# Optimization experiments

Hardware: AMD Instinct MI355X
Metric: run time of the kernel (lower is better)

## Reference

```python
import jax, jax.numpy as jnp
import numpy as np
import math

B, S, D, H, KV, HD = 2, 2048, 2048, 32, 8, 64
N_REP = H // KV


def setup_inputs() -> dict:
    key = jax.random.key(0)
    ks = jax.random.split(key, 6)
    x = jax.random.normal(ks[0], (B, S, D), jnp.float32)
    # torch Linear weights, stored as [in, out] for x @ w
    wq = jax.random.normal(ks[1], (D, H * HD), jnp.float32) * 0.02
    wk = jax.random.normal(ks[2], (D, KV * HD), jnp.float32) * 0.02
    wv = jax.random.normal(ks[3], (D, KV * HD), jnp.float32) * 0.02
    wo = jax.random.normal(ks[4], (H * HD, D), jnp.float32) * 0.02
    # rotary angle table: theta[t, j] = t / 10000^(2j/head_dim)
    inv_freq = 1.0 / (10000.0 ** (jnp.arange(0, HD, 2, dtype=jnp.float32) / HD))
    freqs = jnp.arange(S, dtype=jnp.float32)[:, None] * inv_freq[None, :]  # [S, HD//2]
    mask = jnp.triu(jnp.full((S, S), -1e9, dtype=jnp.float32), k=1)
    return {"x": x, "wq": wq, "wk": wk, "wv": wv, "wo": wo,
            "freqs": freqs, "mask": mask, "start_pos": 0}


def _apply_rope(t, cos, sin):
    # t: [b, s, h, d]; pairs are adjacent (llama complex convention)
    b, s, h, d = t.shape
    t2 = t.reshape(b, s, h, d // 2, 2)
    tr, ti = t2[..., 0], t2[..., 1]
    c = cos[None, :, None, :]
    sn = sin[None, :, None, :]
    out_r = tr * c - ti * sn
    out_i = tr * sn + ti * c
    return jnp.stack([out_r, out_i], axis=-1).reshape(b, s, h, d)


def reference(x, wq, wk, wv, wo, freqs, mask, start_pos):
    bsz, seqlen, _ = x.shape
    cos, sin = jnp.cos(freqs), jnp.sin(freqs)
    xq = (x @ wq).reshape(bsz, seqlen, H, HD)
    xk = (x @ wk).reshape(bsz, seqlen, KV, HD)
    xv = (x @ wv).reshape(bsz, seqlen, KV, HD)
    xq = _apply_rope(xq, cos, sin)
    xk = _apply_rope(xk, cos, sin)
    # start_pos == 0 prefill: cache slice [:start_pos+seqlen] == fresh k/v
    keys = jnp.repeat(xk, N_REP, axis=2)    # [b, s, H, hd]
    values = jnp.repeat(xv, N_REP, axis=2)
    q = xq.transpose(0, 2, 1, 3)            # [b, H, s, hd]
    k = keys.transpose(0, 2, 1, 3)
    v = values.transpose(0, 2, 1, 3)
    scores = jnp.einsum('bhqd,bhkd->bhqk', q, k) / math.sqrt(HD)
    scores = scores + mask[None, None, :, :]
    probs = jax.nn.softmax(scores.astype(jnp.float32), axis=-1).astype(q.dtype)
    out = jnp.einsum('bhqk,bhkd->bhqd', probs, v)
    out = out.transpose(0, 2, 1, 3).reshape(bsz, seqlen, H * HD)
    return out @ wo
```

## Files before the change

### kernel.cpp

```cpp
#include <hip/hip_runtime.h>

typedef __attribute__((ext_vector_type(8))) __bf16 bf16x8;
typedef __attribute__((ext_vector_type(4)))  float f32x4;
typedef __attribute__((ext_vector_type(16))) float f32x16;

__device__ __forceinline__ unsigned short f2bfu(float x) {
  union { float f; unsigned u; } v; v.f = x;
  unsigned r = v.u + 0x7fffu + ((v.u >> 16) & 1u);
  return (unsigned short)(r >> 16);
}
__device__ __forceinline__ float bf2f(unsigned short u) {
  union { unsigned u; float f; } v; v.u = ((unsigned)u) << 16;
  return v.f;
}
__device__ __forceinline__ unsigned pkbf(float a, float b) {
  return (unsigned)f2bfu(a) | ((unsigned)f2bfu(b) << 16);
}
__device__ __forceinline__ void gload16(const void* g, void* l) {
  __builtin_amdgcn_global_load_lds((const __attribute__((address_space(1))) unsigned*)g,
                                   (__attribute__((address_space(3))) unsigned*)l, 16, 0, 0);
}
__device__ __forceinline__ bf16x8 mk8(unsigned a, unsigned b, unsigned c, unsigned d) {
  union { unsigned u[4]; bf16x8 v; } t;
  t.u[0] = a; t.u[1] = b; t.u[2] = c; t.u[3] = d; return t.v;
}

__global__ void cvt_kernel(const float* __restrict__ s, short* __restrict__ d, int n) {
  int i = (blockIdx.x * 256 + threadIdx.x) * 4;
  if (i >= n) return;
  float4 v = *(const float4*)(s + i);
  short4 o;
  o.x = (short)f2bfu(v.x); o.y = (short)f2bfu(v.y);
  o.z = (short)f2bfu(v.z); o.w = (short)f2bfu(v.w);
  *(short4*)(d + i) = o;
}

__global__ void transcvt_kernel(const float* __restrict__ src, short* __restrict__ dst,
                                int R, int C) {
  __shared__ __align__(16) float tl[64][65];
  int c0 = blockIdx.x * 64, r0 = blockIdx.y * 64;
  int t = threadIdx.x;
  int tr = t >> 4, tc = (t & 15) * 4;
#pragma unroll
  for (int i = 0; i < 4; i++) {
    int r = i * 16 + tr;
    float4 v = *(const float4*)(src + (size_t)(r0 + r) * C + c0 + tc);
    tl[r][tc] = v.x; tl[r][tc + 1] = v.y; tl[r][tc + 2] = v.z; tl[r][tc + 3] = v.w;
  }
  __syncthreads();
#pragma unroll
  for (int i = 0; i < 4; i++) {
    int cr = i * 16 + tr;
    short4 o;
    o.x = (short)f2bfu(tl[tc][cr]);
    o.y = (short)f2bfu(tl[tc + 1][cr]);
    o.z = (short)f2bfu(tl[tc + 2][cr]);
    o.w = (short)f2bfu(tl[tc + 3][cr]);
    *(short4*)(dst + (size_t)(c0 + cr) * R + r0 + tc) = o;
  }
}

__global__ void sincos_kernel(const float* __restrict__ freqs, float* __restrict__ ct,
                              float* __restrict__ st) {
  int i = blockIdx.x * 256 + threadIdx.x;
  float f = freqs[i];
  ct[i] = cosf(f);
  st[i] = sinf(f);
}

template <int OUTF32>
__global__ __launch_bounds__(256) void gemm_bt(const short* __restrict__ A,
                                               const short* __restrict__ Bt,
                                               void* __restrict__ C, int M, int N, int K) {
  __shared__ __align__(16) short Al[128 * 32];
  __shared__ __align__(16) short Bl[128 * 32];
  const int t = threadIdx.x, lane = t & 63, w = t >> 6;
  const int m0 = blockIdx.x * 128, n0 = blockIdx.y * 128;
  const int wm = (w & 1) * 64, wn = (w >> 1) * 64;
  f32x4 acc[4][4];
#pragma unroll
  for (int i = 0; i < 4; i++)
#pragma unroll
    for (int j = 0; j < 4; j++)
#pragma unroll
      for (int r = 0; r < 4; r++) acc[i][j][r] = 0.f;

  const int sr = t >> 2;
  const int ss = t & 3;
  const int ldsbase = w * 512;

  for (int k0 = 0; k0 < K; k0 += 32) {
    __syncthreads();
#pragma unroll
    for (int p = 0; p < 2; p++) {
      int r = p * 64 + sr;
      int c = 8 * (ss ^ ((r >> 1) & 3));
      gload16(A + (size_t)(m0 + r) * K + k0 + c, &Al[p * 2048 + ldsbase]);
      gload16(Bt + (size_t)(n0 + r) * K + k0 + c, &Bl[p * 2048 + ldsbase]);
    }
    __syncthreads();
    bf16x8 af[4], bg[4];
#pragma unroll
    for (int i = 0; i < 4; i++) {
      int ra = wm + i * 16 + (lane & 15);
      int sa = (lane >> 4) ^ ((ra >> 1) & 3);
      af[i] = *(const bf16x8*)(&Al[ra * 32 + sa * 8]);
      int rb = wn + i * 16 + (lane & 15);
      int sb = (lane >> 4) ^ ((rb >> 1) & 3);
      bg[i] = *(const bf16x8*)(&Bl[rb * 32 + sb * 8]);
    }
#pragma unroll
    for (int i = 0; i < 4; i++)
#pragma unroll
      for (int j = 0; j < 4; j++)
        acc[i][j] = __builtin_amdgcn_mfma_f32_16x16x32_bf16(af[i], bg[j], acc[i][j], 0, 0, 0);
  }
  const int cr = (lane >> 4) * 4, cc = lane & 15;
#pragma unroll
  for (int i = 0; i < 4; i++)
#pragma unroll
    for (int j = 0; j < 4; j++)
#pragma unroll
      for (int r = 0; r < 4; r++) {
        size_t idx = (size_t)(m0 + wm + i * 16 + cr + r) * N + (n0 + wn + j * 16 + cc);
        if (OUTF32) ((float*)C)[idx] = acc[i][j][r];
        else        ((short*)C)[idx] = (short)f2bfu(acc[i][j][r]);
      }
}

__global__ void rope_kernel(short* __restrict__ qkv, const float* __restrict__ ct,
                            const float* __restrict__ st) {
  int idx = blockIdx.x * 256 + threadIdx.x;
  const int PQ = 4096 * 1024;
  int row, col, i;
  if (idx < PQ) {
    row = idx >> 10; int p = idx & 1023; int h = p >> 5; i = p & 31;
    col = h * 64 + 2 * i;
  } else {
    int k = idx - PQ; row = k >> 8; int p = k & 255; int kvh = p >> 5; i = p & 31;
    col = 2048 + kvh * 64 + 2 * i;
  }
  int s = row & 2047;
  unsigned* ptr = (unsigned*)(qkv + (size_t)row * 3072 + col);
  unsigned v = *ptr;
  float tr = bf2f((unsigned short)(v & 0xffff));
  float ti = bf2f((unsigned short)(v >> 16));
  float c = ct[(s << 5) + i], sn = st[(s << 5) + i];
  *ptr = pkbf(tr * c - ti * sn, tr * sn + ti * c);
}

__global__ void transv_kernel(const short* __restrict__ qkv, short* __restrict__ vt) {
  __shared__ __align__(16) short tl[64][72];
  int st0 = blockIdx.x * 64;
  int bkv = blockIdx.y; int b = bkv >> 3, kv = bkv & 7;
  int t = threadIdx.x;
  int rr = t >> 3, c8 = (t & 7) * 8;
#pragma unroll
  for (int i = 0; i < 2; i++) {
    int sl = i * 32 + rr;
    bf16x8 v = *(const bf16x8*)(qkv + (size_t)(b * 2048 + st0 + sl) * 3072 + 2560 + kv * 64 + c8);
    union { bf16x8 v; short s[8]; } u; u.v = v;
#pragma unroll
    for (int j = 0; j < 8; j++) tl[sl][c8 + j] = u.s[j];
  }
  __syncthreads();
#pragma unroll
  for (int i = 0; i < 2; i++) {
    int dl = i * 32 + rr;
    union { bf16x8 v; short s[8]; } o;
#pragma unroll
    for (int j = 0; j < 8; j++) o.s[j] = tl[c8 + j][dl];
    *(bf16x8*)(vt + ((size_t)(bkv * 64 + dl)) * 2048 + st0 + c8) = o.v;
  }
}

__global__ __launch_bounds__(256) void attn_kernel(const short* __restrict__ qkv,
                                                   const short* __restrict__ vt,
                                                   short* __restrict__ attn) {
  const int S = 2048, NC = 3072;
  __shared__ __align__(16) short kl[32 * 64];
  __shared__ __align__(16) short vl[64 * 32];
  __shared__ __align__(16) short ol[4][32 * 72];

  const int qb = blockIdx.x * 128;
  const int h = blockIdx.y, b = blockIdx.z;
  const int kvh = h >> 2;
  const int t = threadIdx.x, lane = t & 63, w = t >> 6;
  const int q0 = qb + w * 32;
  const int qc = lane & 31, hi = lane >> 5;
  const int qg = q0 + qc;

  bf16x8 bq[4];
  {
    const short* qp = qkv + (size_t)(b * S + qg) * NC + h * 64 + hi * 8;
#pragma unroll
    for (int kk = 0; kk < 4; kk++) bq[kk] = *(const bf16x8*)(qp + kk * 16);
  }

  f32x16 ot0, ot1;
#pragma unroll
  for (int r = 0; r < 16; r++) { ot0[r] = 0.f; ot1[r] = 0.f; }
  float m = -1e30f, l = 0.f;

  const int kr = w * 8 + (lane >> 3), sk = lane & 7;
  const short* kbase = qkv + (size_t)(b * S + kr) * NC + 2048 + kvh * 64 + 8 * (sk ^ (kr & 7));
  const int dv = w * 16 + (lane >> 2), sv = lane & 3;
  const short* vbase = vt + ((size_t)((b * 8 + kvh) * 64 + dv)) * S + 8 * (sv ^ ((dv >> 1) & 3));

  const int nt = (qb >> 5) + 4;
  for (int tile = 0; tile < nt; ++tile) {
    const int s0 = tile * 32;
    __syncthreads();
    gload16(kbase + (size_t)s0 * NC, &kl[w * 512]);
    gload16(vbase + s0, &vl[w * 512]);
    __syncthreads();

    f32x16 cs;
#pragma unroll
    for (int r = 0; r < 16; r++) cs[r] = 0.f;
    const int krow = lane & 31;
#pragma unroll
    for (int kk = 0; kk < 4; kk++) {
      int slot = (2 * kk + hi) ^ (krow & 7);
      bf16x8 ak = *(const bf16x8*)(&kl[krow * 64 + slot * 8]);
      cs = __builtin_amdgcn_mfma_f32_32x32x16_bf16(ak, bq[kk], cs, 0, 0, 0);
    }

    float e[16];
    const bool notfull = (s0 + 31 > q0);
#pragma unroll
    for (int r = 0; r < 16; r++) {
      float sv_ = cs[r] * 0.18033688011112042f;
      if (notfull) {
        int kgl = s0 + (r & 3) + 8 * (r >> 2) + 4 * hi;
        if (kgl > qg) sv_ = -1e30f;
      }
      e[r] = sv_;
    }
    float mx = e[0];
#pragma unroll
    for (int r = 1; r < 16; r++) mx = fmaxf(mx, e[r]);
    mx = fmaxf(mx, __shfl_xor(mx, 32, 64));
    float mn = fmaxf(m, mx);
    float rf = exp2f(m - mn);
    m = mn;
    float p[16]; float ls = 0.f;
#pragma unroll
    for (int r = 0; r < 16; r++) { p[r] = exp2f(e[r] - mn); ls += p[r]; }
    l = l * rf + ls;
#pragma unroll
    for (int r = 0; r < 16; r++) { ot0[r] *= rf; ot1[r] *= rf; }

    unsigned x[8], y[8];
#pragma unroll
    for (int j = 0; j < 8; j++) x[j] = pkbf(p[2 * j], p[2 * j + 1]);
#pragma unroll
    for (int j = 0; j < 8; j++) y[j] = (unsigned)__shfl_xor((int)x[j], 32, 64);
    bf16x8 pb0 = hi ? mk8(y[2], y[3], x[2], x[3]) : mk8(x[0], x[1], y[0], y[1]);
    bf16x8 pb1 = hi ? mk8(y[6], y[7], x[6], x[7]) : mk8(x[4], x[5], y[4], y[5]);

    const int dl = lane & 31;
#pragma unroll
    for (int ks = 0; ks < 2; ks++) {
      bf16x8 pb = ks ? pb1 : pb0;
#pragma unroll
      for (int dh = 0; dh < 2; dh++) {
        int d = dh * 32 + dl;
        int slot = (2 * ks + hi) ^ ((d >> 1) & 3);
        bf16x8 av = *(const bf16x8*)(&vl[d * 32 + slot * 8]);
        if (dh == 0) ot0 = __builtin_amdgcn_mfma_f32_32x32x16_bf16(av, pb, ot0, 0, 0, 0);
        else         ot1 = __builtin_amdgcn_mfma_f32_32x32x16_bf16(av, pb, ot1, 0, 0, 0);
      }
    }
  }

  float lt = l + __shfl_xor(l, 32, 64);
  float inv = 1.0f / lt;
#pragma unroll
  for (int dh = 0; dh < 2; dh++) {
#pragma unroll
    for (int j = 0; j < 8; j++) {
      int d = ((2 * j) & 3) + 8 * ((2 * j) >> 2) + 4 * hi + 32 * dh;
      float a = (dh ? ot1[2 * j] : ot0[2 * j]) * inv;
      float bb = (dh ? ot1[2 * j + 1] : ot0[2 * j + 1]) * inv;
      *(unsigned*)(&ol[w][qc * 72 + d]) = pkbf(a, bb);
    }
  }
  __syncthreads();
  const int qr = lane >> 1, part = lane & 1;
  short* og = attn + (size_t)(b * S + q0 + qr) * 2048 + h * 64 + part * 32;
  const short* ip = &ol[w][qr * 72 + part * 32];
#pragma unroll
  for (int i2 = 0; i2 < 4; i2++) *(bf16x8*)(og + i2 * 8) = *(const bf16x8*)(ip + i2 * 8);
}

extern "C" void kernel_launch(void* const* d_in, const int* in_sizes, int n_in,
                              void* d_out, int out_size, void* d_ws, size_t ws_size,
                              hipStream_t stream) {
  (void)in_sizes; (void)n_in; (void)out_size; (void)ws_size;
  const float* x     = (const float*)d_in[0];
  const float* wq    = (const float*)d_in[1];
  const float* wk    = (const float*)d_in[2];
  const float* wv    = (const float*)d_in[3];
  const float* wo    = (const float*)d_in[4];
  const float* freqs = (const float*)d_in[5];

  char* ws = (char*)d_ws;
  short* qkv  = (short*)(ws + 0);
  short* vtb  = (short*)(ws + 25165824);
  short* xb   = (short*)(ws + 29360128);
  short* attn = xb;
  short* wT   = (short*)(ws + 46137344);
  float* ct   = (float*)(ws + 58720256);
  float* st   = (float*)(ws + 58982400);

  cvt_kernel<<<8192, 256, 0, stream>>>(x, xb, 8388608);
  transcvt_kernel<<<dim3(32, 32), 256, 0, stream>>>(wq, wT, 2048, 2048);
  transcvt_kernel<<<dim3(8, 32), 256, 0, stream>>>(wk, wT + (size_t)2048 * 2048, 2048, 512);
  transcvt_kernel<<<dim3(8, 32), 256, 0, stream>>>(wv, wT + (size_t)2560 * 2048, 2048, 512);
  sincos_kernel<<<256, 256, 0, stream>>>(freqs, ct, st);
  gemm_bt<0><<<dim3(32, 24), 256, 0, stream>>>(xb, wT, qkv, 4096, 3072, 2048);
  transcvt_kernel<<<dim3(32, 32), 256, 0, stream>>>(wo, wT, 2048, 2048);
  rope_kernel<<<20480, 256, 0, stream>>>(qkv, ct, st);
  transv_kernel<<<dim3(32, 16), 256, 0, stream>>>(qkv, vtb);
  attn_kernel<<<dim3(16, 32, 2), 256, 0, stream>>>(qkv, vtb, attn);
  gemm_bt<1><<<dim3(32, 16), 256, 0, stream>>>(attn, wT, d_out, 4096, 2048, 2048);
}
```

Baseline: 473.9 us.

## Double-buffer 64-key K/V tiles in attention with prescaled Q and reversed block order

The attention loop now processes 64 keys per iteration instead of 32 and double-buffers K/V tiles in shared memory, so the next tile's global-to-LDS loads overlap with the current tile's MFMA work. The softmax scale is folded into Q once at load time rather than applied per score. Query blocks are launched in reverse order so the longest causal blocks start first, and bf16 packing uses the native conversion. The cost is more LDS per block, which may lower occupancy, and scaling Q before the bf16 round adds a small rounding change.

```diff
diff --git a/kernel.cpp b/kernel.cpp
--- a/kernel.cpp
+++ b/kernel.cpp
@@ -15,6 +15,11 @@
 }
 __device__ __forceinline__ unsigned pkbf(float a, float b) {
   return (unsigned)f2bfu(a) | ((unsigned)f2bfu(b) << 16);
+}
+__device__ __forceinline__ unsigned pk2(float a, float b) {
+  union { __bf16 h[2]; unsigned u; } t;
+  t.h[0] = (__bf16)a; t.h[1] = (__bf16)b;
+  return t.u;
 }
 __device__ __forceinline__ void gload16(const void* g, void* l) {
   __builtin_amdgcn_global_load_lds((const __attribute__((address_space(1))) unsigned*)g,
@@ -178,11 +183,9 @@
                                                    const short* __restrict__ vt,
                                                    short* __restrict__ attn) {
   const int S = 2048, NC = 3072;
-  __shared__ __align__(16) short kl[32 * 64];
-  __shared__ __align__(16) short vl[64 * 32];
-  __shared__ __align__(16) short ol[4][32 * 72];
-
-  const int qb = blockIdx.x * 128;
+  __shared__ __align__(16) short sh[2][2][64 * 64];
+
+  const int qb = (int)(gridDim.x - 1 - blockIdx.x) * 128;
   const int h = blockIdx.y, b = blockIdx.z;
   const int kvh = h >> 2;
   const int t = threadIdx.x, lane = t & 63, w = t >> 6;
@@ -193,8 +196,15 @@
   bf16x8 bq[4];
   {
     const short* qp = qkv + (size_t)(b * S + qg) * NC + h * 64 + hi * 8;
-#pragma unroll
-    for (int kk = 0; kk < 4; kk++) bq[kk] = *(const bf16x8*)(qp + kk * 16);
+    const float SC = 0.18033688011112042f;
+#pragma unroll
+    for (int kk = 0; kk < 4; kk++) {
+      union { bf16x8 v; unsigned short s[8]; } u, o;
+      u.v = *(const bf16x8*)(qp + kk * 16);
+#pragma unroll
+      for (int j = 0; j < 8; j++) o.s[j] = f2bfu(bf2f(u.s[j]) * SC);
+      bq[kk] = o.v;
+    }
   }
 
   f32x16 ot0, ot1;
@@ -202,78 +212,115 @@
   for (int r = 0; r < 16; r++) { ot0[r] = 0.f; ot1[r] = 0.f; }
   float m = -1e30f, l = 0.f;
 
-  const int kr = w * 8 + (lane >> 3), sk = lane & 7;
-  const short* kbase = qkv + (size_t)(b * S + kr) * NC + 2048 + kvh * 64 + 8 * (sk ^ (kr & 7));
-  const int dv = w * 16 + (lane >> 2), sv = lane & 3;
-  const short* vbase = vt + ((size_t)((b * 8 + kvh) * 64 + dv)) * S + 8 * (sv ^ ((dv >> 1) & 3));
-
-  const int nt = (qb >> 5) + 4;
-  for (int tile = 0; tile < nt; ++tile) {
-    const int s0 = tile * 32;
+  const int r8 = lane >> 3, sl8 = lane & 7;
+  const int scol0 = 8 * (sl8 ^ ((r8 + w) & 7));
+  const int scol1 = 8 * (sl8 ^ ((r8 + 4 + w) & 7));
+  const short* kptr = qkv + (size_t)(b * S + w * 8 + r8) * NC + 2048 + kvh * 64;
+  const short* vptr = vt + (size_t)((b * 8 + kvh) * 64 + w * 8 + r8) * S;
+
+  const int nt = (qb >> 6) + 2;
+
+#define STAGE(tt, bb)                                                                   \
+  do {                                                                                  \
+    gload16(kptr + (size_t)((tt) * 64) * NC + scol0,        &sh[bb][0][(w * 8) * 64]);  \
+    gload16(kptr + (size_t)((tt) * 64 + 32) * NC + scol1,   &sh[bb][0][(32 + w * 8) * 64]); \
+    gload16(vptr + (size_t)(tt) * 64 + scol0,               &sh[bb][1][(w * 8) * 64]);  \
+    gload16(vptr + (size_t)32 * S + (tt) * 64 + scol1,      &sh[bb][1][(32 + w * 8) * 64]); \
+  } while (0)
+
+  STAGE(0, 0);
+  __syncthreads();
+
+  for (int tt = 0; tt < nt; ++tt) {
+    const int cur = tt & 1;
+    if (tt + 1 < nt) STAGE(tt + 1, cur ^ 1);
+    const int s0 = tt * 64;
+    const short* kb = &sh[cur][0][0];
+    const short* vb = &sh[cur][1][0];
+
+    f32x16 cs0, cs1;
+#pragma unroll
+    for (int r = 0; r < 16; r++) { cs0[r] = 0.f; cs1[r] = 0.f; }
+    const int kr0 = lane & 31, kr1 = kr0 + 32;
+    const int sw0 = (kr0 + (kr0 >> 3)) & 7, sw1 = (kr1 + (kr1 >> 3)) & 7;
+#pragma unroll
+    for (int kk = 0; kk < 4; kk++) {
+      bf16x8 a0 = *(const bf16x8*)(kb + kr0 * 64 + ((2 * kk + hi) ^ sw0) * 8);
+      cs0 = __builtin_amdgcn_mfma_f32_32x32x16_bf16(a0, bq[kk], cs0, 0, 0, 0);
+      bf16x8 a1 = *(const bf16x8*)(kb + kr1 * 64 + ((2 * kk + hi) ^ sw1) * 8);
+      cs1 = __builtin_amdgcn_mfma_f32_32x32x16_bf16(a1, bq[kk], cs1, 0, 0, 0);
+    }
+
+    if (s0 + 63 > q0) {
+      const int qrel = qg - s0;
+#pragma unroll
+      for (int r = 0; r < 16; r++) {
+        const int k0 = (r & 3) + 8 * (r >> 2) + 4 * hi;
+        if (k0 > qrel)      cs0[r] = -1e30f;
+        if (k0 + 32 > qrel) cs1[r] = -1e30f;
+      }
+    }
+
+    float mx = fmaxf(cs0[0], cs1[0]);
+#pragma unroll
+    for (int r = 1; r < 16; r++) mx = fmaxf(mx, fmaxf(cs0[r], cs1[r]));
+    mx = fmaxf(mx, __shfl_xor(mx, 32, 64));
+    const float mn = fmaxf(m, mx);
+    const float rf = exp2f(m - mn);
+    m = mn;
+    float ls = 0.f;
+#pragma unroll
+    for (int r = 0; r < 16; r++) { cs0[r] = exp2f(cs0[r] - mn); ls += cs0[r]; }
+#pragma unroll
+    for (int r = 0; r < 16; r++) { cs1[r] = exp2f(cs1[r] - mn); ls += cs1[r]; }
+    l = l * rf + ls;
+#pragma unroll
+    for (int r = 0; r < 16; r++) { ot0[r] *= rf; ot1[r] *= rf; }
+
+    unsigned x0[8], y0[8], x1[8], y1[8];
+#pragma unroll
+    for (int j = 0; j < 8; j++) x0[j] = pk2(cs0[2 * j], cs0[2 * j + 1]);
+#pragma unroll
+    for (int j = 0; j < 8; j++) y0[j] = (unsigned)__shfl_xor((int)x0[j], 32, 64);
+#pragma unroll
+    for (int j = 0; j < 8; j++) x1[j] = pk2(cs1[2 * j], cs1[2 * j + 1]);
+#pragma unroll
+    for (int j = 0; j < 8; j++) y1[j] = (unsigned)__shfl_xor((int)x1[j], 32, 64);
+    bf16x8 pb0 = hi ? mk8(y0[2], y0[3], x0[2], x0[3]) : mk8(x0[0], x0[1], y0[0], y0[1]);
+    bf16x8 pb1 = hi ? mk8(y0[6], y0[7], x0[6], x0[7]) : mk8(x0[4], x0[5], y0[4], y0[5]);
+    bf16x8 pb2 = hi ? mk8(y1[2], y1[3], x1[2], x1[3]) : mk8(x1[0], x1[1], y1[0], y1[1]);
+    bf16x8 pb3 = hi ? mk8(y1[6], y1[7], x1[6], x1[7]) : mk8(x1[4], x1[5], y1[4], y1[5]);
+
+    const int dl = lane & 31;
+    {
+      const int d = dl;
+      const int swd = (d + (d >> 3)) & 7;
+      bf16x8 v0 = *(const bf16x8*)(vb + d * 64 + ((0 + hi) ^ swd) * 8);
+      bf16x8 v1 = *(const bf16x8*)(vb + d * 64 + ((2 + hi) ^ swd) * 8);
+      bf16x8 v2 = *(const bf16x8*)(vb + d * 64 + ((4 + hi) ^ swd) * 8);
+      bf16x8 v3 = *(const bf16x8*)(vb + d * 64 + ((6 + hi) ^ swd) * 8);
+      ot0 = __builtin_amdgcn_mfma_f32_32x32x16_bf16(v0, pb0, ot0, 0, 0, 0);
+      ot0 = __builtin_amdgcn_mfma_f32_32x32x16_bf16(v1, pb1, ot0, 0, 0, 0);
+      ot0 = __builtin_amdgcn_mfma_f32_32x32x16_bf16(v2, pb2, ot0, 0, 0, 0);
+      ot0 = __builtin_amdgcn_mfma_f32_32x32x16_bf16(v3, pb3, ot0, 0, 0, 0);
+    }
+    {
+      const int d = 32 + dl;
+      const int swd = (d + (d >> 3)) & 7;
+      bf16x8 v0 = *(const bf16x8*)(vb + d * 64 + ((0 + hi) ^ swd) * 8);
+      bf16x8 v1 = *(const bf16x8*)(vb + d * 64 + ((2 + hi) ^ swd) * 8);
+      bf16x8 v2 = *(const bf16x8*)(vb + d * 64 + ((4 + hi) ^ swd) * 8);
+      bf16x8 v3 = *(const bf16x8*)(vb + d * 64 + ((6 + hi) ^ swd) * 8);
+      ot1 = __builtin_amdgcn_mfma_f32_32x32x16_bf16(v0, pb0, ot1, 0, 0, 0);
+      ot1 = __builtin_amdgcn_mfma_f32_32x32x16_bf16(v1, pb1, ot1, 0, 0, 0);
+      ot1 = __builtin_amdgcn_mfma_f32_32x32x16_bf16(v2, pb2, ot1, 0, 0, 0);
+      ot1 = __builtin_amdgcn_mfma_f32_32x32x16_bf16(v3, pb3, ot1, 0, 0, 0);
+    }
     __syncthreads();
-    gload16(kbase + (size_t)s0 * NC, &kl[w * 512]);
-    gload16(vbase + s0, &vl[w * 512]);
-    __syncthreads();
-
-    f32x16 cs;
-#pragma unroll
-    for (int r = 0; r < 16; r++) cs[r] = 0.f;
-    const int krow = lane & 31;
-#pragma unroll
-    for (int kk = 0; kk < 4; kk++) {
-      int slot = (2 * kk + hi) ^ (krow & 7);
-      bf16x8 ak = *(const bf16x8*)(&kl[krow * 64 + slot * 8]);
-      cs = __builtin_amdgcn_mfma_f32_32x32x16_bf16(ak, bq[kk], cs, 0, 0, 0);
-    }
-
-    float e[16];
-    const bool notfull = (s0 + 31 > q0);
-#pragma unroll
-    for (int r = 0; r < 16; r++) {
-      float sv_ = cs[r] * 0.18033688011112042f;
-      if (notfull) {
-        int kgl = s0 + (r & 3) + 8 * (r >> 2) + 4 * hi;
-        if (kgl > qg) sv_ = -1e30f;
-      }
-      e[r] = sv_;
-    }
-    float mx = e[0];
-#pragma unroll
-    for (int r = 1; r < 16; r++) mx = fmaxf(mx, e[r]);
-    mx = fmaxf(mx, __shfl_xor(mx, 32, 64));
-    float mn = fmaxf(m, mx);
-    float rf = exp2f(m - mn);
-    m = mn;
-    float p[16]; float ls = 0.f;
-#pragma unroll
-    for (int r = 0; r < 16; r++) { p[r] = exp2f(e[r] - mn); ls += p[r]; }
-    l = l * rf + ls;
-#pragma unroll
-    for (int r = 0; r < 16; r++) { ot0[r] *= rf; ot1[r] *= rf; }
-
-    unsigned x[8], y[8];
-#pragma unroll
-    for (int j = 0; j < 8; j++) x[j] = pkbf(p[2 * j], p[2 * j + 1]);
-#pragma unroll
-    for (int j = 0; j < 8; j++) y[j] = (unsigned)__shfl_xor((int)x[j], 32, 64);
-    bf16x8 pb0 = hi ? mk8(y[2], y[3], x[2], x[3]) : mk8(x[0], x[1], y[0], y[1]);
-    bf16x8 pb1 = hi ? mk8(y[6], y[7], x[6], x[7]) : mk8(x[4], x[5], y[4], y[5]);
-
-    const int dl = lane & 31;
-#pragma unroll
-    for (int ks = 0; ks < 2; ks++) {
-      bf16x8 pb = ks ? pb1 : pb0;
-#pragma unroll
-      for (int dh = 0; dh < 2; dh++) {
-        int d = dh * 32 + dl;
-        int slot = (2 * ks + hi) ^ ((d >> 1) & 3);
-        bf16x8 av = *(const bf16x8*)(&vl[d * 32 + slot * 8]);
-        if (dh == 0) ot0 = __builtin_amdgcn_mfma_f32_32x32x16_bf16(av, pb, ot0, 0, 0, 0);
-        else         ot1 = __builtin_amdgcn_mfma_f32_32x32x16_bf16(av, pb, ot1, 0, 0, 0);
-      }
-    }
-  }
-
+  }
+#undef STAGE
+
+  short (*ol)[32 * 72] = (short (*)[32 * 72]) & sh[0][0][0];
   float lt = l + __shfl_xor(l, 32, 64);
   float inv = 1.0f / lt;
 #pragma unroll
```

Result: faster. 440.6 us (-7.0%).
